# Kernel tuning notes

Measured on AMD Instinct MI355X. Metric: run time of the kernel, lower is better.

Reference implementation:

```python
import jax, jax.numpy as jnp
import numpy as np

# static config (levels=4, CDA=False branch -> self_attn_4, scale=4, f=False)
SHAPES = [(80, 80), (40, 40), (20, 20), (10, 10)]
D = 256; NH = 8; NL = 4; NP = 4; DFF = 1024; DH = D // NH
L = sum(h * w for h, w in SHAPES)  # 8500
B = 1


def layer_norm(x, g, b, eps=1e-5):
    m = jnp.mean(x, axis=-1, keepdims=True)
    v = jnp.mean((x - m) ** 2, axis=-1, keepdims=True)
    return (x - m) * jax.lax.rsqrt(v + eps) * g + b


def ms_deform_attn_core(value, loc, attn):
    # value: [B, L, NH, DH]; loc: [B, Lq, NH, NL, NP, 2] in [0,1]; attn: [B, Lq, NH, NL, NP]
    Bq, Lq = loc.shape[0], loc.shape[1]
    out = jnp.zeros((Bq, NH, Lq, DH), value.dtype)
    start = 0
    for lvl, (Hl, Wl) in enumerate(SHAPES):
        v = value[:, start:start + Hl * Wl]          # [B, HW, NH, DH]
        start += Hl * Wl
        v = v.transpose(0, 2, 1, 3)                  # [B, NH, HW, DH]
        ll = loc[:, :, :, lvl]                       # [B, Lq, NH, NP, 2]
        # grid_sample semantics: align_corners=False, padding_mode='zeros'
        x = ll[..., 0] * Wl - 0.5
        y = ll[..., 1] * Hl - 0.5
        x0 = jnp.floor(x); y0 = jnp.floor(y)
        acc = jnp.zeros((Bq, NH, Lq, NP, DH), value.dtype)
        for dy in (0, 1):
            for dx in (0, 1):
                xi = x0 + dx; yi = y0 + dy
                w = (1.0 - jnp.abs(x - xi)) * (1.0 - jnp.abs(y - yi))  # [B,Lq,NH,NP]
                valid = (xi >= 0) & (xi < Wl) & (yi >= 0) & (yi < Hl)
                xi_c = jnp.clip(xi, 0, Wl - 1).astype(jnp.int32)
                yi_c = jnp.clip(yi, 0, Hl - 1).astype(jnp.int32)
                lin = (yi_c * Wl + xi_c).transpose(0, 2, 1, 3).reshape(Bq, NH, Lq * NP)
                g = jnp.take_along_axis(v, lin[..., None], axis=2).reshape(Bq, NH, Lq, NP, DH)
                wv = (w * valid.astype(w.dtype)).transpose(0, 2, 1, 3)[..., None]
                acc = acc + g * wv
        aw = attn[:, :, :, lvl].transpose(0, 2, 1, 3)[..., None]  # [B,NH,Lq,NP,1]
        out = out + jnp.sum(acc * aw, axis=3)
    return out.transpose(0, 2, 1, 3).reshape(Bq, Lq, NH * DH)


def setup_inputs():
    key = jax.random.key(0)
    ks = jax.random.split(key, 24)
    s = 0.02
    d = {}
    d['src'] = jax.random.normal(ks[0], (B, L, D), jnp.float32)
    d['pos'] = jax.random.normal(ks[1], (B, L, D), jnp.float32)
    d['reference_points'] = jax.random.uniform(ks[2], (B, L, NL, 2), jnp.float32)
    d['spatial_shapes'] = jnp.array(SHAPES, jnp.int32)
    d['level_start_index'] = jnp.array(np.cumsum([0] + [h * w for h, w in SHAPES[:-1]]), jnp.int32)
    d['scale'] = 4
    # MSDeformAttn params
    d['Wo'] = jax.random.normal(ks[3], (D, NH * NL * NP * 2), jnp.float32) * s
    d['bo'] = jax.random.normal(ks[4], (NH * NL * NP * 2,), jnp.float32) * s
    d['Wa'] = jax.random.normal(ks[5], (D, NH * NL * NP), jnp.float32) * s
    d['ba'] = jax.random.normal(ks[6], (NH * NL * NP,), jnp.float32) * s
    d['Wv'] = jax.random.normal(ks[7], (D, D), jnp.float32) * s
    d['bv'] = jnp.zeros((D,), jnp.float32)
    d['Wout'] = jax.random.normal(ks[8], (D, D), jnp.float32) * s
    d['bout'] = jnp.zeros((D,), jnp.float32)
    # FFN + LayerNorms
    d['W1'] = jax.random.normal(ks[9], (D, DFF), jnp.float32) * s
    d['b1'] = jnp.zeros((DFF,), jnp.float32)
    d['W2'] = jax.random.normal(ks[10], (DFF, D), jnp.float32) * s
    d['b2'] = jnp.zeros((D,), jnp.float32)
    d['g1'] = jnp.ones((D,), jnp.float32); d['be1'] = jnp.zeros((D,), jnp.float32)
    d['g2'] = jnp.ones((D,), jnp.float32); d['be2'] = jnp.zeros((D,), jnp.float32)
    return d


def reference(src, pos, reference_points, spatial_shapes, level_start_index, scale,
              Wo, bo, Wa, ba, Wv, bv, Wout, bout, W1, b1, W2, b2, g1, be1, g2, be2):
    Bq, Lq, _ = src.shape
    q = src + pos  # with_pos_embed
    # sampling offsets & attention weights (softmax over levels*points)
    off = (q @ Wo + bo).reshape(Bq, Lq, NH, NL, NP, 2)
    attn = jax.nn.softmax((q @ Wa + ba).reshape(Bq, Lq, NH, NL * NP), axis=-1)
    attn = attn.reshape(Bq, Lq, NH, NL, NP)
    value = (src @ Wv + bv).reshape(Bq, L, NH, DH)
    # offset normalizer is (W, H) per level
    normalizer = jnp.stack([spatial_shapes[:, 1], spatial_shapes[:, 0]], -1).astype(src.dtype)
    loc = reference_points[:, :, None, :, None, :] + off / normalizer[None, None, None, :, None, :]
    src2 = ms_deform_attn_core(value, loc, attn) @ Wout + bout
    # residual + norm1 (dropout = eval identity)
    x = layer_norm(src + src2, g1, be1)
    # FFN
    ffn = jax.nn.relu(x @ W1 + b1) @ W2 + b2
    x = layer_norm(x + ffn, g2, be2)
    return x
```

## Files before the change

### kernel.cpp

```cpp
#include <hip/hip_runtime.h>
#include <hip/hip_bf16.h>
#include <string.h>

#define D 256
#define NH 8
#define DH 32
#define NL 4
#define NP 4
#define DFF 1024
#define LTOT 8500

typedef __bf16 bf16x8 __attribute__((ext_vector_type(8)));
typedef float floatx4 __attribute__((ext_vector_type(4)));

__device__ inline unsigned bpack(float a, float b) {
    __hip_bfloat16 ha = __float2bfloat16(a), hb = __float2bfloat16(b);
    unsigned short ua, ub;
    memcpy(&ua, &ha, 2); memcpy(&ub, &hb, 2);
    return (unsigned)ua | ((unsigned)ub << 16);
}

__device__ inline void gload16(const void* g, void* l) {
    __builtin_amdgcn_global_load_lds((const __attribute__((address_space(1))) void*)g,
                                     (__attribute__((address_space(3))) void*)l,
                                     16, 0, 0);
}

__global__ void transpose_all(const float* W0, const float* W1_, const float* W2_,
                              const float* W3, const float* W4, const float* W5,
                              __hip_bfloat16* T0, __hip_bfloat16* T1, __hip_bfloat16* T2,
                              __hip_bfloat16* T3, __hip_bfloat16* T4, __hip_bfloat16* T5,
                              const float* src, const float* pos,
                              __hip_bfloat16* qb, __hip_bfloat16* srcb) {
    int id = blockIdx.x;
    if (id >= 736) {
        int idx = (id - 736) * 2048 + threadIdx.x * 8;
        if (idx < LTOT * 256) {
            float4 s0 = *(const float4*)(src + idx);
            float4 s1 = *(const float4*)(src + idx + 4);
            float4 p0 = *(const float4*)(pos + idx);
            float4 p1 = *(const float4*)(pos + idx + 4);
            uint4 us, uq;
            us.x = bpack(s0.x, s0.y); us.y = bpack(s0.z, s0.w);
            us.z = bpack(s1.x, s1.y); us.w = bpack(s1.z, s1.w);
            uq.x = bpack(s0.x + p0.x, s0.y + p0.y); uq.y = bpack(s0.z + p0.z, s0.w + p0.w);
            uq.z = bpack(s1.x + p1.x, s1.y + p1.y); uq.w = bpack(s1.z + p1.z, s1.w + p1.w);
            *(uint4*)(srcb + idx) = us;
            *(uint4*)(qb + idx)  = uq;
        }
        return;
    }
    const int cum[7] = {0, 64, 96, 160, 224, 480, 736};
    int mi = 0;
    while (id >= cum[mi + 1]) mi++;
    int lid = id - cum[mi];
    const float* W; __hip_bfloat16* T; int K, N;
    switch (mi) {
        case 0: W = W0; T = T0; K = 256;  N = 256;  break;
        case 1: W = W1_; T = T1; K = 256; N = 128;  break;
        case 2: W = W2_; T = T2; K = 256; N = 256;  break;
        case 3: W = W3; T = T3; K = 256;  N = 256;  break;
        case 4: W = W4; T = T4; K = 256;  N = 1024; break;
        default: W = W5; T = T5; K = 1024; N = 256; break;
    }
    int ntx = N >> 5;
    int n0 = (lid % ntx) * 32, k0 = (lid / ntx) * 32;
    __shared__ float t[32][33];
    int tx = threadIdx.x & 31, ty = threadIdx.x >> 5;
#pragma unroll
    for (int i = 0; i < 32; i += 8)
        t[ty + i][tx] = W[(size_t)(k0 + ty + i) * N + n0 + tx];
    __syncthreads();
#pragma unroll
    for (int i = 0; i < 32; i += 8)
        T[(size_t)(n0 + ty + i) * K + k0 + tx] = __float2bfloat16(t[tx][ty + i]);
}

__global__ __launch_bounds__(256) void gemm_t(
    const __hip_bfloat16* __restrict__ A, const __hip_bfloat16* __restrict__ BT,
    const float* __restrict__ bias, float* __restrict__ Cf, __hip_bfloat16* __restrict__ Cb,
    int M, int N, int K, int relu) {
    constexpr int BM = 64, BN = 64, BK = 64;
    __shared__ __align__(16) __hip_bfloat16 sA[BM * BK];
    __shared__ __align__(16) __hip_bfloat16 sB[BN * BK];

    int tid = threadIdx.x, wave = tid >> 6, lane = tid & 63;
    int m0 = blockIdx.y * BM, n0 = blockIdx.x * BN;
    int wm = (wave >> 1) * 32, wn = (wave & 1) * 32;

    floatx4 acc[2][2];
#pragma unroll
    for (int i = 0; i < 2; i++)
#pragma unroll
        for (int j = 0; j < 2; j++)
#pragma unroll
            for (int e = 0; e < 4; e++) acc[i][j][e] = 0.f;

    int lrow = lane & 15, swz = lrow & 7;
    int scol = ((lane & 7) ^ (lane >> 3)) << 3;

    const __hip_bfloat16* aP[2];
    const __hip_bfloat16* bP[2];
#pragma unroll
    for (int i = 0; i < 2; i++) {
        int ra = m0 + i * 32 + wave * 8 + (lane >> 3); if (ra >= M) ra = M - 1;
        aP[i] = A + (size_t)ra * K + scol;
        int rb = n0 + i * 32 + wave * 8 + (lane >> 3);
        bP[i] = BT + (size_t)rb * K + scol;
    }
    int dOff = wave * 1024 + lane * 16;

    for (int k0 = 0; k0 < K; k0 += BK) {
#pragma unroll
        for (int i = 0; i < 2; i++) gload16(aP[i] + k0, (char*)sA + i * 4096 + dOff);
#pragma unroll
        for (int i = 0; i < 2; i++) gload16(bP[i] + k0, (char*)sB + i * 4096 + dOff);
        __syncthreads();
#pragma unroll
        for (int kk = 0; kk < 2; kk++) {
            int co = (((kk << 2) + (lane >> 4)) ^ swz) << 3;
            bf16x8 af[2], bfr[2];
#pragma unroll
            for (int tm = 0; tm < 2; tm++)
                af[tm] = *(const bf16x8*)(&sA[(wm + tm * 16 + lrow) * BK + co]);
#pragma unroll
            for (int tn = 0; tn < 2; tn++)
                bfr[tn] = *(const bf16x8*)(&sB[(wn + tn * 16 + lrow) * BK + co]);
#pragma unroll
            for (int tm = 0; tm < 2; tm++)
#pragma unroll
                for (int tn = 0; tn < 2; tn++)
                    acc[tm][tn] = __builtin_amdgcn_mfma_f32_16x16x32_bf16(af[tm], bfr[tn], acc[tm][tn], 0, 0, 0);
        }
        __syncthreads();
    }

    int lcol = lane & 15, lr4 = (lane >> 4) * 4;
#pragma unroll
    for (int tm = 0; tm < 2; tm++) {
#pragma unroll
        for (int i = 0; i < 4; i++) {
            int row = m0 + wm + tm * 16 + lr4 + i;
            if (row < M) {
#pragma unroll
                for (int tn = 0; tn < 2; tn++) {
                    int col = n0 + wn + tn * 16 + lcol;
                    float v = acc[tm][tn][i] + bias[col];
                    if (relu) v = fmaxf(v, 0.f);
                    if (Cf) Cf[(size_t)row * N + col] = v;
                    if (Cb) Cb[(size_t)row * N + col] = __float2bfloat16(v);
                }
            }
        }
    }
}

__global__ __launch_bounds__(256) void proj2(
    const __hip_bfloat16* __restrict__ qb, const __hip_bfloat16* __restrict__ srcb,
    const __hip_bfloat16* __restrict__ WoT, const __hip_bfloat16* __restrict__ WaT,
    const __hip_bfloat16* __restrict__ WvT,
    const float* __restrict__ bo, const float* __restrict__ ba, const float* __restrict__ bv,
    float* __restrict__ locb, float* __restrict__ attnb, __hip_bfloat16* __restrict__ valb,
    int M) {
    constexpr int BM = 64, BN = 64, BK = 64, K = 256;
    __shared__ __align__(16) __hip_bfloat16 sA[BM * BK];
    __shared__ __align__(16) __hip_bfloat16 sB[BN * BK];

    int n0 = blockIdx.x * BN;
    int m0 = blockIdx.y * BM;

    const __hip_bfloat16* BT;
    const __hip_bfloat16* A;
    const float* bias;
    int ncol0, Nout;
    float* Cf; __hip_bfloat16* Cb;
    if (n0 < 256)      { A = qb;   BT = WoT; bias = bo; ncol0 = n0;       Nout = 256; Cf = locb;  Cb = nullptr; }
    else if (n0 < 384) { A = qb;   BT = WaT; bias = ba; ncol0 = n0 - 256; Nout = 128; Cf = attnb; Cb = nullptr; }
    else               { A = srcb; BT = WvT; bias = bv; ncol0 = n0 - 384; Nout = 256; Cf = nullptr; Cb = valb; }

    int tid = threadIdx.x, wave = tid >> 6, lane = tid & 63;
    int wm = (wave >> 1) * 32, wn = (wave & 1) * 32;

    floatx4 acc[2][2];
#pragma unroll
    for (int i = 0; i < 2; i++)
#pragma unroll
        for (int j = 0; j < 2; j++)
#pragma unroll
            for (int e = 0; e < 4; e++) acc[i][j][e] = 0.f;

    int lrow = lane & 15, swz = lrow & 7;
    int scol = ((lane & 7) ^ (lane >> 3)) << 3;

    const __hip_bfloat16* aP[2];
    const __hip_bfloat16* bP[2];
#pragma unroll
    for (int i = 0; i < 2; i++) {
        int ra = m0 + i * 32 + wave * 8 + (lane >> 3); if (ra >= M) ra = M - 1;
        aP[i] = A + (size_t)ra * K + scol;
        int rb = ncol0 + i * 32 + wave * 8 + (lane >> 3);
        bP[i] = BT + (size_t)rb * K + scol;
    }
    int dOff = wave * 1024 + lane * 16;

    for (int k0 = 0; k0 < K; k0 += BK) {
#pragma unroll
        for (int i = 0; i < 2; i++) gload16(aP[i] + k0, (char*)sA + i * 4096 + dOff);
#pragma unroll
        for (int i = 0; i < 2; i++) gload16(bP[i] + k0, (char*)sB + i * 4096 + dOff);
        __syncthreads();
#pragma unroll
        for (int kk = 0; kk < 2; kk++) {
            int co = (((kk << 2) + (lane >> 4)) ^ swz) << 3;
            bf16x8 af[2], bfr[2];
#pragma unroll
            for (int tm = 0; tm < 2; tm++)
                af[tm] = *(const bf16x8*)(&sA[(wm + tm * 16 + lrow) * BK + co]);
#pragma unroll
            for (int tn = 0; tn < 2; tn++)
                bfr[tn] = *(const bf16x8*)(&sB[(wn + tn * 16 + lrow) * BK + co]);
#pragma unroll
            for (int tm = 0; tm < 2; tm++)
#pragma unroll
                for (int tn = 0; tn < 2; tn++)
                    acc[tm][tn] = __builtin_amdgcn_mfma_f32_16x16x32_bf16(af[tm], bfr[tn], acc[tm][tn], 0, 0, 0);
        }
        __syncthreads();
    }

    int lcol = lane & 15, lr4 = (lane >> 4) * 4;
#pragma unroll
    for (int tm = 0; tm < 2; tm++) {
#pragma unroll
        for (int i = 0; i < 4; i++) {
            int row = m0 + wm + tm * 16 + lr4 + i;
            if (row < M) {
#pragma unroll
                for (int tn = 0; tn < 2; tn++) {
                    int col = ncol0 + wn + tn * 16 + lcol;
                    float v = acc[tm][tn][i] + bias[col];
                    if (Cf) Cf[(size_t)row * Nout + col] = v;
                    else    Cb[(size_t)row * Nout + col] = __float2bfloat16(v);
                }
            }
        }
    }
}

__global__ __launch_bounds__(256) void deform(const __hip_bfloat16* __restrict__ value,
                                              const float* __restrict__ locraw,
                                              const float* __restrict__ logits,
                                              const float* __restrict__ refp,
                                              __hip_bfloat16* __restrict__ out) {
    __shared__ float wS[4][8][16][4];
    __shared__ int   aS[4][8][16][4];
    int tid = threadIdx.x;
    int q0 = blockIdx.x * 4;

    {
        int sub = tid >> 6, h = (tid >> 3) & 7, t8 = tid & 7;
        int q = q0 + sub;
        const float* lg = logits + q * 128 + h * 16;
        float l0 = lg[t8], l1 = lg[t8 + 8];
        float mx = fmaxf(l0, l1);
#pragma unroll
        for (int m = 1; m < 8; m <<= 1) mx = fmaxf(mx, __shfl_xor(mx, m, 64));
        float e0 = __expf(l0 - mx), e1 = __expf(l1 - mx);
        float s = e0 + e1;
#pragma unroll
        for (int m = 1; m < 8; m <<= 1) s += __shfl_xor(s, m, 64);
        float inv = 1.f / s;

        const int starts[4] = {0, 6400, 8000, 8400};
#pragma unroll
        for (int j = 0; j < 2; j++) {
            int pp = t8 + 8 * j;
            float a = (j ? e1 : e0) * inv;
            int l = pp >> 2;
            int Wl = 80 >> l;
            float nv = (float)Wl;
            float rx = refp[q * 8 + l * 2 + 0];
            float ry = refp[q * 8 + l * 2 + 1];
            float lx = rx + locraw[q * 256 + h * 32 + pp * 2 + 0] / nv;
            float ly = ry + locraw[q * 256 + h * 32 + pp * 2 + 1] / nv;
            float x = lx * nv - 0.5f;
            float y = ly * nv - 0.5f;
            float x0f = floorf(x), y0f = floorf(y);
            float fx = x - x0f, fy = y - y0f;
            int x0 = (int)x0f, y0 = (int)y0f;
            float wts[4] = {(1.f - fx) * (1.f - fy), fx * (1.f - fy),
                            (1.f - fx) * fy,         fx * fy};
            int st = starts[l];
#pragma unroll
            for (int t = 0; t < 4; t++) {
                int xi = x0 + (t & 1), yi = y0 + (t >> 1);
                bool valid = (xi >= 0) & (xi < Wl) & (yi >= 0) & (yi < Wl);
                int xc = min(max(xi, 0), Wl - 1), yc = min(max(yi, 0), Wl - 1);
                wS[sub][h][pp][t] = valid ? wts[t] * a : 0.f;
                aS[sub][h][pp][t] = (st + yc * Wl + xc) * 512 + h * 64;
            }
        }
    }
    __syncthreads();

    int sub = tid >> 6, h = (tid >> 3) & 7, l8 = tid & 7;
    int q = q0 + sub;
    const char* vb = (const char*)value;
    int lo = l8 * 8;
    float a0 = 0.f, a1 = 0.f, a2 = 0.f, a3 = 0.f;
#pragma unroll
    for (int p = 0; p < 16; p++) {
        floatx4 w = *(const floatx4*)&wS[sub][h][p][0];
        int4 av = *(const int4*)&aS[sub][h][p][0];
#pragma unroll
        for (int t = 0; t < 4; t++) {
            int ad = (t == 0) ? av.x : (t == 1) ? av.y : (t == 2) ? av.z : av.w;
            uint2 u = *(const uint2*)(vb + ad + lo);
            float wt = w[t];
            a0 += wt * __uint_as_float(u.x << 16);
            a1 += wt * __uint_as_float(u.x & 0xffff0000u);
            a2 += wt * __uint_as_float(u.y << 16);
            a3 += wt * __uint_as_float(u.y & 0xffff0000u);
        }
    }
    uint2 o;
    o.x = bpack(a0, a1);
    o.y = bpack(a2, a3);
    *(uint2*)((char*)out + q * 512 + h * 64 + l8 * 8) = o;
}

__global__ __launch_bounds__(512) void gemm_ln(
    const __hip_bfloat16* __restrict__ A, const __hip_bfloat16* __restrict__ BT,
    const float* __restrict__ bias, const float* __restrict__ resid,
    const float* __restrict__ g, const float* __restrict__ be,
    float* __restrict__ outf, __hip_bfloat16* __restrict__ outb,
    int M, int K) {
    constexpr int BM = 16, BK = 64;
    __shared__ __align__(16) __hip_bfloat16 sA[BM * BK];
    __shared__ __align__(16) __hip_bfloat16 sB[256 * BK];
    __shared__ float psum[8][16], psq[8][16], mS[16], rS[16];

    int tid = threadIdx.x;
    int wave = tid >> 6, lane = tid & 63;
    int m0 = blockIdx.x * BM;

    floatx4 acc[2];
#pragma unroll
    for (int j = 0; j < 2; j++)
#pragma unroll
        for (int e = 0; e < 4; e++) acc[j][e] = 0.f;

    int lrow = lane & 15, swz = lrow & 7;

    int scolA = ((lane & 7) ^ (lane >> 3)) << 3;
    int grA = m0 + wave * 8 + (lane >> 3); if (grA >= M) grA = M - 1;
    const __hip_bfloat16* aP = A + (size_t)grA * K + scolA;

    int scolB = ((tid & 7) ^ ((tid >> 3) & 7)) << 3;
    const __hip_bfloat16* bP[4];
#pragma unroll
    for (int i = 0; i < 4; i++)
        bP[i] = BT + (size_t)(i * 64 + (tid >> 3)) * K + scolB;

    for (int k0 = 0; k0 < K; k0 += BK) {
        if (wave < 2) gload16(aP + k0, (char*)sA + wave * 1024 + lane * 16);
#pragma unroll
        for (int i = 0; i < 4; i++) gload16(bP[i] + k0, (char*)sB + i * 8192 + tid * 16);
        __syncthreads();
#pragma unroll
        for (int kk = 0; kk < 2; kk++) {
            int co = (((kk << 2) + (lane >> 4)) ^ swz) << 3;
            bf16x8 af, bfr[2];
            af = *(const bf16x8*)(&sA[lrow * BK + co]);
#pragma unroll
            for (int tn = 0; tn < 2; tn++)
                bfr[tn] = *(const bf16x8*)(&sB[(wave * 32 + tn * 16 + lrow) * BK + co]);
#pragma unroll
            for (int tn = 0; tn < 2; tn++)
                acc[tn] = __builtin_amdgcn_mfma_f32_16x16x32_bf16(af, bfr[tn], acc[tn], 0, 0, 0);
        }
        __syncthreads();
    }

    int lcol = lane & 15, quad = lane >> 4;
    float v[2][4];
#pragma unroll
    for (int i = 0; i < 4; i++) {
        int row = quad * 4 + i;
        int grow = m0 + row; if (grow >= M) grow = M - 1;
#pragma unroll
        for (int tn = 0; tn < 2; tn++) {
            int col = wave * 32 + tn * 16 + lcol;
            v[tn][i] = acc[tn][i] + bias[col] + resid[(size_t)grow * 256 + col];
        }
    }

#pragma unroll
    for (int i = 0; i < 4; i++) {
        float s = 0.f, s2 = 0.f;
#pragma unroll
        for (int tn = 0; tn < 2; tn++) { float x = v[tn][i]; s += x; s2 += x * x; }
#pragma unroll
        for (int m = 1; m < 16; m <<= 1) {
            s  += __shfl_xor(s, m, 64);
            s2 += __shfl_xor(s2, m, 64);
        }
        if (lcol == 0) {
            int row = quad * 4 + i;
            psum[wave][row] = s;
            psq[wave][row]  = s2;
        }
    }
    __syncthreads();
    if (tid < 16) {
        float s = 0.f, s2 = 0.f;
#pragma unroll
        for (int w = 0; w < 8; w++) { s += psum[w][tid]; s2 += psq[w][tid]; }
        float m = s * (1.f / 256.f);
        float var = fmaxf(s2 * (1.f / 256.f) - m * m, 0.f);
        mS[tid] = m;
        rS[tid] = rsqrtf(var + 1e-5f);
    }
    __syncthreads();

#pragma unroll
    for (int i = 0; i < 4; i++) {
        int row = quad * 4 + i;
        int grow = m0 + row;
        if (grow < M) {
            float m = mS[row], r = rS[row];
#pragma unroll
            for (int tn = 0; tn < 2; tn++) {
                int col = wave * 32 + tn * 16 + lcol;
                float o = (v[tn][i] - m) * r * g[col] + be[col];
                outf[(size_t)grow * 256 + col] = o;
                if (outb) outb[(size_t)grow * 256 + col] = __float2bfloat16(o);
            }
        }
    }
}

extern "C" void kernel_launch(void* const* d_in, const int* in_sizes, int n_in,
                              void* d_out, int out_size, void* d_ws, size_t ws_size,
                              hipStream_t stream) {
    const float* src  = (const float*)d_in[0];
    const float* pos  = (const float*)d_in[1];
    const float* refp = (const float*)d_in[2];
    const float* Wo   = (const float*)d_in[6];
    const float* bo   = (const float*)d_in[7];
    const float* Wa   = (const float*)d_in[8];
    const float* ba   = (const float*)d_in[9];
    const float* Wv   = (const float*)d_in[10];
    const float* bv   = (const float*)d_in[11];
    const float* Wout = (const float*)d_in[12];
    const float* bout = (const float*)d_in[13];
    const float* W1   = (const float*)d_in[14];
    const float* b1   = (const float*)d_in[15];
    const float* W2   = (const float*)d_in[16];
    const float* b2   = (const float*)d_in[17];
    const float* g1   = (const float*)d_in[18];
    const float* be1  = (const float*)d_in[19];
    const float* g2   = (const float*)d_in[20];
    const float* be2  = (const float*)d_in[21];
    float* out = (float*)d_out;
    char* ws = (char*)d_ws;

    __hip_bfloat16* WoT   = (__hip_bfloat16*)(ws + 0);
    __hip_bfloat16* WaT   = (__hip_bfloat16*)(ws + 131072);
    __hip_bfloat16* WvT   = (__hip_bfloat16*)(ws + 196608);
    __hip_bfloat16* WoutT = (__hip_bfloat16*)(ws + 327680);
    __hip_bfloat16* W1T   = (__hip_bfloat16*)(ws + 458752);
    __hip_bfloat16* W2T   = (__hip_bfloat16*)(ws + 983040);
    float*          locb  = (float*)(ws + 1507328);
    float*          attnb = (float*)(ws + 10211328);
    __hip_bfloat16* valb  = (__hip_bfloat16*)(ws + 14563328);
    __hip_bfloat16* aob   = (__hip_bfloat16*)(ws + 18915328);
    float*          x1    = (float*)(ws + 23267328);
    __hip_bfloat16* x1b   = (__hip_bfloat16*)(ws + 31971328);
    __hip_bfloat16* hb    = (__hip_bfloat16*)(ws + 36323328);
    __hip_bfloat16* qb    = (__hip_bfloat16*)(ws + 36323328);
    __hip_bfloat16* srcb  = (__hip_bfloat16*)(ws + 36323328 + 4352000);

    transpose_all<<<736 + 1063, 256, 0, stream>>>(Wo, Wa, Wv, Wout, W1, W2,
                                                  WoT, WaT, WvT, WoutT, W1T, W2T,
                                                  src, pos, qb, srcb);

    proj2<<<dim3(10, 133), 256, 0, stream>>>(qb, srcb, WoT, WaT, WvT, bo, ba, bv,
                                             locb, attnb, valb, LTOT);

    deform<<<2125, 256, 0, stream>>>(valb, locb, attnb, refp, aob);

    gemm_ln<<<532, 512, 0, stream>>>(aob, WoutT, bout, src, g1, be1, x1, x1b, LTOT, 256);

    gemm_t<<<dim3(16, 133), 256, 0, stream>>>(x1b, W1T, b1, nullptr, hb, LTOT, 1024, 256, 1);

    gemm_ln<<<532, 512, 0, stream>>>(hb, W2T, b2, x1, g2, be2, out, nullptr, LTOT, 1024);
}
```

Measured before the change: 197.0 us.

## Fuse all stages into one cooperative persistent kernel with grid syncs

Replaces the six separate launches (transpose/convert, projection GEMM, deformable sampling, two GEMM+LayerNorm stages and the FFN GEMM) with a single cooperative kernel of 512-thread blocks. Stages are separated by grid.sync and blocks loop over work units. GEMM tiles change to 64x128 with 8 waves. The aim is to remove launch overhead and inter-kernel gaps. In exchange, grid-wide barriers, occupancy limited by the shared-memory union, and grid-stride imbalance may cost more than the launches they replace.

```diff
diff --git a/kernel.cpp b/kernel.cpp
--- a/kernel.cpp
+++ b/kernel.cpp
@@ -1,6 +1,9 @@
 #include <hip/hip_runtime.h>
 #include <hip/hip_bf16.h>
+#include <hip/hip_cooperative_groups.h>
 #include <string.h>
+
+namespace cg = cooperative_groups;
 
 #define D 256
 #define NH 8
@@ -26,67 +29,24 @@
                                      16, 0, 0);
 }
 
-__global__ void transpose_all(const float* W0, const float* W1_, const float* W2_,
-                              const float* W3, const float* W4, const float* W5,
-                              __hip_bfloat16* T0, __hip_bfloat16* T1, __hip_bfloat16* T2,
-                              __hip_bfloat16* T3, __hip_bfloat16* T4, __hip_bfloat16* T5,
-                              const float* src, const float* pos,
-                              __hip_bfloat16* qb, __hip_bfloat16* srcb) {
-    int id = blockIdx.x;
-    if (id >= 736) {
-        int idx = (id - 736) * 2048 + threadIdx.x * 8;
-        if (idx < LTOT * 256) {
-            float4 s0 = *(const float4*)(src + idx);
-            float4 s1 = *(const float4*)(src + idx + 4);
-            float4 p0 = *(const float4*)(pos + idx);
-            float4 p1 = *(const float4*)(pos + idx + 4);
-            uint4 us, uq;
-            us.x = bpack(s0.x, s0.y); us.y = bpack(s0.z, s0.w);
-            us.z = bpack(s1.x, s1.y); us.w = bpack(s1.z, s1.w);
-            uq.x = bpack(s0.x + p0.x, s0.y + p0.y); uq.y = bpack(s0.z + p0.z, s0.w + p0.w);
-            uq.z = bpack(s1.x + p1.x, s1.y + p1.y); uq.w = bpack(s1.z + p1.z, s1.w + p1.w);
-            *(uint4*)(srcb + idx) = us;
-            *(uint4*)(qb + idx)  = uq;
-        }
-        return;
-    }
-    const int cum[7] = {0, 64, 96, 160, 224, 480, 736};
-    int mi = 0;
-    while (id >= cum[mi + 1]) mi++;
-    int lid = id - cum[mi];
-    const float* W; __hip_bfloat16* T; int K, N;
-    switch (mi) {
-        case 0: W = W0; T = T0; K = 256;  N = 256;  break;
-        case 1: W = W1_; T = T1; K = 256; N = 128;  break;
-        case 2: W = W2_; T = T2; K = 256; N = 256;  break;
-        case 3: W = W3; T = T3; K = 256;  N = 256;  break;
-        case 4: W = W4; T = T4; K = 256;  N = 1024; break;
-        default: W = W5; T = T5; K = 1024; N = 256; break;
-    }
-    int ntx = N >> 5;
-    int n0 = (lid % ntx) * 32, k0 = (lid / ntx) * 32;
-    __shared__ float t[32][33];
-    int tx = threadIdx.x & 31, ty = threadIdx.x >> 5;
-#pragma unroll
-    for (int i = 0; i < 32; i += 8)
-        t[ty + i][tx] = W[(size_t)(k0 + ty + i) * N + n0 + tx];
-    __syncthreads();
-#pragma unroll
-    for (int i = 0; i < 32; i += 8)
-        T[(size_t)(n0 + ty + i) * K + k0 + tx] = __float2bfloat16(t[tx][ty + i]);
-}
-
-__global__ __launch_bounds__(256) void gemm_t(
-    const __hip_bfloat16* __restrict__ A, const __hip_bfloat16* __restrict__ BT,
-    const float* __restrict__ bias, float* __restrict__ Cf, __hip_bfloat16* __restrict__ Cb,
-    int M, int N, int K, int relu) {
-    constexpr int BM = 64, BN = 64, BK = 64;
-    __shared__ __align__(16) __hip_bfloat16 sA[BM * BK];
-    __shared__ __align__(16) __hip_bfloat16 sB[BN * BK];
-
+__device__ void gemm_64x128(char* smem,
+                            const __hip_bfloat16* A, const __hip_bfloat16* BT,
+                            int m0, int bRow0, int K, int M,
+                            const float* bias, int colOff, int ldOut,
+                            float* Cf, __hip_bfloat16* Cb, int relu) {
+    __hip_bfloat16* sA = (__hip_bfloat16*)smem;
+    __hip_bfloat16* sB = (__hip_bfloat16*)(smem + 8192);
     int tid = threadIdx.x, wave = tid >> 6, lane = tid & 63;
-    int m0 = blockIdx.y * BM, n0 = blockIdx.x * BN;
-    int wm = (wave >> 1) * 32, wn = (wave & 1) * 32;
+    int wm = (wave >> 2) * 32, wn = (wave & 3) * 32;
+    int lrow = lane & 15, swz = lrow & 7;
+    int scol = ((tid & 7) ^ ((tid >> 3) & 7)) << 3;
+
+    int ra = m0 + (tid >> 3); if (ra >= M) ra = M - 1;
+    const __hip_bfloat16* aP = A + (size_t)ra * K + scol;
+    const __hip_bfloat16* bP[2];
+#pragma unroll
+    for (int i = 0; i < 2; i++)
+        bP[i] = BT + (size_t)(bRow0 + i * 64 + (tid >> 3)) * K + scol;
 
     floatx4 acc[2][2];
 #pragma unroll
@@ -96,25 +56,11 @@
 #pragma unroll
             for (int e = 0; e < 4; e++) acc[i][j][e] = 0.f;
 
-    int lrow = lane & 15, swz = lrow & 7;
-    int scol = ((lane & 7) ^ (lane >> 3)) << 3;
-
-    const __hip_bfloat16* aP[2];
-    const __hip_bfloat16* bP[2];
-#pragma unroll
-    for (int i = 0; i < 2; i++) {
-        int ra = m0 + i * 32 + wave * 8 + (lane >> 3); if (ra >= M) ra = M - 1;
-        aP[i] = A + (size_t)ra * K + scol;
-        int rb = n0 + i * 32 + wave * 8 + (lane >> 3);
-        bP[i] = BT + (size_t)rb * K + scol;
-    }
-    int dOff = wave * 1024 + lane * 16;
-
-    for (int k0 = 0; k0 < K; k0 += BK) {
-#pragma unroll
-        for (int i = 0; i < 2; i++) gload16(aP[i] + k0, (char*)sA + i * 4096 + dOff);
-#pragma unroll
-        for (int i = 0; i < 2; i++) gload16(bP[i] + k0, (char*)sB + i * 4096 + dOff);
+    for (int k0 = 0; k0 < K; k0 += 64) {
+        gload16(aP + k0, smem + tid * 16);
+#pragma unroll
+        for (int i = 0; i < 2; i++)
+            gload16(bP[i] + k0, smem + 8192 + (i * 512 + tid) * 16);
         __syncthreads();
 #pragma unroll
         for (int kk = 0; kk < 2; kk++) {
@@ -122,10 +68,10 @@
             bf16x8 af[2], bfr[2];
 #pragma unroll
             for (int tm = 0; tm < 2; tm++)
-                af[tm] = *(const bf16x8*)(&sA[(wm + tm * 16 + lrow) * BK + co]);
+                af[tm] = *(const bf16x8*)(&sA[(wm + tm * 16 + lrow) * 64 + co]);
 #pragma unroll
             for (int tn = 0; tn < 2; tn++)
-                bfr[tn] = *(const bf16x8*)(&sB[(wn + tn * 16 + lrow) * BK + co]);
+                bfr[tn] = *(const bf16x8*)(&sB[(wn + tn * 16 + lrow) * 64 + co]);
 #pragma unroll
             for (int tm = 0; tm < 2; tm++)
 #pragma unroll
@@ -144,213 +90,38 @@
             if (row < M) {
 #pragma unroll
                 for (int tn = 0; tn < 2; tn++) {
-                    int col = n0 + wn + tn * 16 + lcol;
-                    float v = acc[tm][tn][i] + bias[col];
+                    int c = wn + tn * 16 + lcol;
+                    float v = acc[tm][tn][i] + bias[colOff + c];
                     if (relu) v = fmaxf(v, 0.f);
-                    if (Cf) Cf[(size_t)row * N + col] = v;
-                    if (Cb) Cb[(size_t)row * N + col] = __float2bfloat16(v);
+                    if (Cf) Cf[(size_t)row * ldOut + colOff + c] = v;
+                    else    Cb[(size_t)row * ldOut + colOff + c] = __float2bfloat16(v);
                 }
             }
         }
     }
 }
 
-__global__ __launch_bounds__(256) void proj2(
-    const __hip_bfloat16* __restrict__ qb, const __hip_bfloat16* __restrict__ srcb,
-    const __hip_bfloat16* __restrict__ WoT, const __hip_bfloat16* __restrict__ WaT,
-    const __hip_bfloat16* __restrict__ WvT,
-    const float* __restrict__ bo, const float* __restrict__ ba, const float* __restrict__ bv,
-    float* __restrict__ locb, float* __restrict__ attnb, __hip_bfloat16* __restrict__ valb,
-    int M) {
-    constexpr int BM = 64, BN = 64, BK = 64, K = 256;
-    __shared__ __align__(16) __hip_bfloat16 sA[BM * BK];
-    __shared__ __align__(16) __hip_bfloat16 sB[BN * BK];
-
-    int n0 = blockIdx.x * BN;
-    int m0 = blockIdx.y * BM;
-
-    const __hip_bfloat16* BT;
-    const __hip_bfloat16* A;
-    const float* bias;
-    int ncol0, Nout;
-    float* Cf; __hip_bfloat16* Cb;
-    if (n0 < 256)      { A = qb;   BT = WoT; bias = bo; ncol0 = n0;       Nout = 256; Cf = locb;  Cb = nullptr; }
-    else if (n0 < 384) { A = qb;   BT = WaT; bias = ba; ncol0 = n0 - 256; Nout = 128; Cf = attnb; Cb = nullptr; }
-    else               { A = srcb; BT = WvT; bias = bv; ncol0 = n0 - 384; Nout = 256; Cf = nullptr; Cb = valb; }
+__device__ void gemm_ln_dev(char* smem,
+                            const __hip_bfloat16* A, const __hip_bfloat16* BT,
+                            const float* bias, const float* resid,
+                            const float* g, const float* be,
+                            float* outf, __hip_bfloat16* outb,
+                            int m0, int M, int K) {
+    __hip_bfloat16* sA = (__hip_bfloat16*)smem;
+    __hip_bfloat16* sB = (__hip_bfloat16*)(smem + 2048);
+    float* psum = (float*)(smem + 34816);
+    float* psq  = (float*)(smem + 35328);
+    float* mS   = (float*)(smem + 35840);
+    float* rS   = (float*)(smem + 35904);
 
     int tid = threadIdx.x, wave = tid >> 6, lane = tid & 63;
-    int wm = (wave >> 1) * 32, wn = (wave & 1) * 32;
-
-    floatx4 acc[2][2];
-#pragma unroll
-    for (int i = 0; i < 2; i++)
-#pragma unroll
-        for (int j = 0; j < 2; j++)
-#pragma unroll
-            for (int e = 0; e < 4; e++) acc[i][j][e] = 0.f;
-
     int lrow = lane & 15, swz = lrow & 7;
-    int scol = ((lane & 7) ^ (lane >> 3)) << 3;
-
-    const __hip_bfloat16* aP[2];
-    const __hip_bfloat16* bP[2];
-#pragma unroll
-    for (int i = 0; i < 2; i++) {
-        int ra = m0 + i * 32 + wave * 8 + (lane >> 3); if (ra >= M) ra = M - 1;
-        aP[i] = A + (size_t)ra * K + scol;
-        int rb = ncol0 + i * 32 + wave * 8 + (lane >> 3);
-        bP[i] = BT + (size_t)rb * K + scol;
-    }
-    int dOff = wave * 1024 + lane * 16;
-
-    for (int k0 = 0; k0 < K; k0 += BK) {
-#pragma unroll
-        for (int i = 0; i < 2; i++) gload16(aP[i] + k0, (char*)sA + i * 4096 + dOff);
-#pragma unroll
-        for (int i = 0; i < 2; i++) gload16(bP[i] + k0, (char*)sB + i * 4096 + dOff);
-        __syncthreads();
-#pragma unroll
-        for (int kk = 0; kk < 2; kk++) {
-            int co = (((kk << 2) + (lane >> 4)) ^ swz) << 3;
-            bf16x8 af[2], bfr[2];
-#pragma unroll
-            for (int tm = 0; tm < 2; tm++)
-                af[tm] = *(const bf16x8*)(&sA[(wm + tm * 16 + lrow) * BK + co]);
-#pragma unroll
-            for (int tn = 0; tn < 2; tn++)
-                bfr[tn] = *(const bf16x8*)(&sB[(wn + tn * 16 + lrow) * BK + co]);
-#pragma unroll
-            for (int tm = 0; tm < 2; tm++)
-#pragma unroll
-                for (int tn = 0; tn < 2; tn++)
-                    acc[tm][tn] = __builtin_amdgcn_mfma_f32_16x16x32_bf16(af[tm], bfr[tn], acc[tm][tn], 0, 0, 0);
-        }
-        __syncthreads();
-    }
-
-    int lcol = lane & 15, lr4 = (lane >> 4) * 4;
-#pragma unroll
-    for (int tm = 0; tm < 2; tm++) {
-#pragma unroll
-        for (int i = 0; i < 4; i++) {
-            int row = m0 + wm + tm * 16 + lr4 + i;
-            if (row < M) {
-#pragma unroll
-                for (int tn = 0; tn < 2; tn++) {
-                    int col = ncol0 + wn + tn * 16 + lcol;
-                    float v = acc[tm][tn][i] + bias[col];
-                    if (Cf) Cf[(size_t)row * Nout + col] = v;
-                    else    Cb[(size_t)row * Nout + col] = __float2bfloat16(v);
-                }
-            }
-        }
-    }
-}
-
-__global__ __launch_bounds__(256) void deform(const __hip_bfloat16* __restrict__ value,
-                                              const float* __restrict__ locraw,
-                                              const float* __restrict__ logits,
-                                              const float* __restrict__ refp,
-                                              __hip_bfloat16* __restrict__ out) {
-    __shared__ float wS[4][8][16][4];
-    __shared__ int   aS[4][8][16][4];
-    int tid = threadIdx.x;
-    int q0 = blockIdx.x * 4;
-
-    {
-        int sub = tid >> 6, h = (tid >> 3) & 7, t8 = tid & 7;
-        int q = q0 + sub;
-        const float* lg = logits + q * 128 + h * 16;
-        float l0 = lg[t8], l1 = lg[t8 + 8];
-        float mx = fmaxf(l0, l1);
-#pragma unroll
-        for (int m = 1; m < 8; m <<= 1) mx = fmaxf(mx, __shfl_xor(mx, m, 64));
-        float e0 = __expf(l0 - mx), e1 = __expf(l1 - mx);
-        float s = e0 + e1;
-#pragma unroll
-        for (int m = 1; m < 8; m <<= 1) s += __shfl_xor(s, m, 64);
-        float inv = 1.f / s;
-
-        const int starts[4] = {0, 6400, 8000, 8400};
-#pragma unroll
-        for (int j = 0; j < 2; j++) {
-            int pp = t8 + 8 * j;
-            float a = (j ? e1 : e0) * inv;
-            int l = pp >> 2;
-            int Wl = 80 >> l;
-            float nv = (float)Wl;
-            float rx = refp[q * 8 + l * 2 + 0];
-            float ry = refp[q * 8 + l * 2 + 1];
-            float lx = rx + locraw[q * 256 + h * 32 + pp * 2 + 0] / nv;
-            float ly = ry + locraw[q * 256 + h * 32 + pp * 2 + 1] / nv;
-            float x = lx * nv - 0.5f;
-            float y = ly * nv - 0.5f;
-            float x0f = floorf(x), y0f = floorf(y);
-            float fx = x - x0f, fy = y - y0f;
-            int x0 = (int)x0f, y0 = (int)y0f;
-            float wts[4] = {(1.f - fx) * (1.f - fy), fx * (1.f - fy),
-                            (1.f - fx) * fy,         fx * fy};
-            int st = starts[l];
-#pragma unroll
-            for (int t = 0; t < 4; t++) {
-                int xi = x0 + (t & 1), yi = y0 + (t >> 1);
-                bool valid = (xi >= 0) & (xi < Wl) & (yi >= 0) & (yi < Wl);
-                int xc = min(max(xi, 0), Wl - 1), yc = min(max(yi, 0), Wl - 1);
-                wS[sub][h][pp][t] = valid ? wts[t] * a : 0.f;
-                aS[sub][h][pp][t] = (st + yc * Wl + xc) * 512 + h * 64;
-            }
-        }
-    }
-    __syncthreads();
-
-    int sub = tid >> 6, h = (tid >> 3) & 7, l8 = tid & 7;
-    int q = q0 + sub;
-    const char* vb = (const char*)value;
-    int lo = l8 * 8;
-    float a0 = 0.f, a1 = 0.f, a2 = 0.f, a3 = 0.f;
-#pragma unroll
-    for (int p = 0; p < 16; p++) {
-        floatx4 w = *(const floatx4*)&wS[sub][h][p][0];
-        int4 av = *(const int4*)&aS[sub][h][p][0];
-#pragma unroll
-        for (int t = 0; t < 4; t++) {
-            int ad = (t == 0) ? av.x : (t == 1) ? av.y : (t == 2) ? av.z : av.w;
-            uint2 u = *(const uint2*)(vb + ad + lo);
-            float wt = w[t];
-            a0 += wt * __uint_as_float(u.x << 16);
-            a1 += wt * __uint_as_float(u.x & 0xffff0000u);
-            a2 += wt * __uint_as_float(u.y << 16);
-            a3 += wt * __uint_as_float(u.y & 0xffff0000u);
-        }
-    }
-    uint2 o;
-    o.x = bpack(a0, a1);
-    o.y = bpack(a2, a3);
-    *(uint2*)((char*)out + q * 512 + h * 64 + l8 * 8) = o;
-}
-
-__global__ __launch_bounds__(512) void gemm_ln(
-    const __hip_bfloat16* __restrict__ A, const __hip_bfloat16* __restrict__ BT,
-    const float* __restrict__ bias, const float* __restrict__ resid,
-    const float* __restrict__ g, const float* __restrict__ be,
-    float* __restrict__ outf, __hip_bfloat16* __restrict__ outb,
-    int M, int K) {
-    constexpr int BM = 16, BK = 64;
-    __shared__ __align__(16) __hip_bfloat16 sA[BM * BK];
-    __shared__ __align__(16) __hip_bfloat16 sB[256 * BK];
-    __shared__ float psum[8][16], psq[8][16], mS[16], rS[16];
-
-    int tid = threadIdx.x;
-    int wave = tid >> 6, lane = tid & 63;
-    int m0 = blockIdx.x * BM;
 
     floatx4 acc[2];
 #pragma unroll
     for (int j = 0; j < 2; j++)
 #pragma unroll
         for (int e = 0; e < 4; e++) acc[j][e] = 0.f;
-
-    int lrow = lane & 15, swz = lrow & 7;
 
     int scolA = ((lane & 7) ^ (lane >> 3)) << 3;
     int grA = m0 + wave * 8 + (lane >> 3); if (grA >= M) grA = M - 1;
@@ -362,19 +133,20 @@
     for (int i = 0; i < 4; i++)
         bP[i] = BT + (size_t)(i * 64 + (tid >> 3)) * K + scolB;
 
-    for (int k0 = 0; k0 < K; k0 += BK) {
-        if (wave < 2) gload16(aP + k0, (char*)sA + wave * 1024 + lane * 16);
-#pragma unroll
-        for (int i = 0; i < 4; i++) gload16(bP[i] + k0, (char*)sB + i * 8192 + tid * 16);
+    for (int k0 = 0; k0 < K; k0 += 64) {
+        if (wave < 2) gload16(aP + k0, smem + wave * 1024 + lane * 16);
+#pragma unroll
+        for (int i = 0; i < 4; i++)
+            gload16(bP[i] + k0, smem + 2048 + i * 8192 + tid * 16);
         __syncthreads();
 #pragma unroll
         for (int kk = 0; kk < 2; kk++) {
             int co = (((kk << 2) + (lane >> 4)) ^ swz) << 3;
-            bf16x8 af, bfr[2];
-            af = *(const bf16x8*)(&sA[lrow * BK + co]);
+            bf16x8 af = *(const bf16x8*)(&sA[lrow * 64 + co]);
+            bf16x8 bfr[2];
 #pragma unroll
             for (int tn = 0; tn < 2; tn++)
-                bfr[tn] = *(const bf16x8*)(&sB[(wave * 32 + tn * 16 + lrow) * BK + co]);
+                bfr[tn] = *(const bf16x8*)(&sB[(wave * 32 + tn * 16 + lrow) * 64 + co]);
 #pragma unroll
             for (int tn = 0; tn < 2; tn++)
                 acc[tn] = __builtin_amdgcn_mfma_f32_16x16x32_bf16(af, bfr[tn], acc[tn], 0, 0, 0);
@@ -407,15 +179,15 @@
         }
         if (lcol == 0) {
             int row = quad * 4 + i;
-            psum[wave][row] = s;
-            psq[wave][row]  = s2;
+            psum[wave * 16 + row] = s;
+            psq[wave * 16 + row]  = s2;
         }
     }
     __syncthreads();
     if (tid < 16) {
         float s = 0.f, s2 = 0.f;
 #pragma unroll
-        for (int w = 0; w < 8; w++) { s += psum[w][tid]; s2 += psq[w][tid]; }
+        for (int w = 0; w < 8; w++) { s += psum[w * 16 + tid]; s2 += psq[w * 16 + tid]; }
         float m = s * (1.f / 256.f);
         float var = fmaxf(s2 * (1.f / 256.f) - m * m, 0.f);
         mS[tid] = m;
@@ -438,6 +210,184 @@
             }
         }
     }
+    __syncthreads();
+}
+
+__global__ void mega(
+    const float* src, const float* pos, const float* refp,
+    const float* Wo, const float* bo, const float* Wa, const float* ba,
+    const float* Wv, const float* bv, const float* Wout, const float* bout,
+    const float* W1, const float* b1, const float* W2, const float* b2,
+    const float* g1, const float* be1, const float* g2, const float* be2,
+    float* out, char* ws) {
+    __shared__ __align__(16) char smem[35968];
+    int tid = threadIdx.x;
+    cg::grid_group grid = cg::this_grid();
+
+    __hip_bfloat16* WoT   = (__hip_bfloat16*)(ws + 0);
+    __hip_bfloat16* WaT   = (__hip_bfloat16*)(ws + 131072);
+    __hip_bfloat16* WvT   = (__hip_bfloat16*)(ws + 196608);
+    __hip_bfloat16* WoutT = (__hip_bfloat16*)(ws + 327680);
+    __hip_bfloat16* W1T   = (__hip_bfloat16*)(ws + 458752);
+    __hip_bfloat16* W2T   = (__hip_bfloat16*)(ws + 983040);
+    float*          locb  = (float*)(ws + 1507328);
+    float*          attnb = (float*)(ws + 10211328);
+    __hip_bfloat16* valb  = (__hip_bfloat16*)(ws + 14563328);
+    __hip_bfloat16* aob   = (__hip_bfloat16*)(ws + 18915328);
+    float*          x1    = (float*)(ws + 23267328);
+    __hip_bfloat16* x1b   = (__hip_bfloat16*)(ws + 31971328);
+    __hip_bfloat16* qb    = (__hip_bfloat16*)(ws + 36323328);
+    __hip_bfloat16* srcb  = (__hip_bfloat16*)(ws + 40675328);
+    __hip_bfloat16* hb    = (__hip_bfloat16*)(ws + 45027328);
+
+    for (int u = blockIdx.x; u < 1268; u += gridDim.x) {
+        if (u < 736) {
+            const int cum[7] = {0, 64, 96, 160, 224, 480, 736};
+            int mi = 0;
+            while (u >= cum[mi + 1]) mi++;
+            int lid = u - cum[mi];
+            const float* W; __hip_bfloat16* T; int K, N;
+            switch (mi) {
+                case 0: W = Wo;   T = WoT;   K = 256;  N = 256;  break;
+                case 1: W = Wa;   T = WaT;   K = 256;  N = 128;  break;
+                case 2: W = Wv;   T = WvT;   K = 256;  N = 256;  break;
+                case 3: W = Wout; T = WoutT; K = 256;  N = 256;  break;
+                case 4: W = W1;   T = W1T;   K = 256;  N = 1024; break;
+                default: W = W2;  T = W2T;   K = 1024; N = 256;  break;
+            }
+            int ntx = N >> 5;
+            int n0 = (lid % ntx) * 32, k0 = (lid / ntx) * 32;
+            float* t = (float*)smem;
+            int tx = tid & 31, ty = tid >> 5;
+#pragma unroll
+            for (int i = 0; i < 32; i += 16)
+                t[(ty + i) * 33 + tx] = W[(size_t)(k0 + ty + i) * N + n0 + tx];
+            __syncthreads();
+#pragma unroll
+            for (int i = 0; i < 32; i += 16)
+                T[(size_t)(n0 + ty + i) * K + k0 + tx] = __float2bfloat16(t[tx * 33 + ty + i]);
+            __syncthreads();
+        } else {
+            int idx = (u - 736) * 4096 + tid * 8;
+            if (idx < LTOT * 256) {
+                float4 s0 = *(const float4*)(src + idx);
+                float4 s1 = *(const float4*)(src + idx + 4);
+                float4 p0 = *(const float4*)(pos + idx);
+                float4 p1 = *(const float4*)(pos + idx + 4);
+                uint4 us, uq;
+                us.x = bpack(s0.x, s0.y); us.y = bpack(s0.z, s0.w);
+                us.z = bpack(s1.x, s1.y); us.w = bpack(s1.z, s1.w);
+                uq.x = bpack(s0.x + p0.x, s0.y + p0.y); uq.y = bpack(s0.z + p0.z, s0.w + p0.w);
+                uq.z = bpack(s1.x + p1.x, s1.y + p1.y); uq.w = bpack(s1.z + p1.z, s1.w + p1.w);
+                *(uint4*)(srcb + idx) = us;
+                *(uint4*)(qb + idx)  = uq;
+            }
+        }
+    }
+    grid.sync();
+
+    for (int u = blockIdx.x; u < 665; u += gridDim.x) {
+        int n0 = (u % 5) * 128, m0 = (u / 5) * 64;
+        const __hip_bfloat16* Ap; const __hip_bfloat16* BTp;
+        const float* bias; int ncol0, Nout; float* Cf; __hip_bfloat16* Cb;
+        if (n0 < 256)      { Ap = qb;   BTp = WoT; bias = bo; ncol0 = n0;       Nout = 256; Cf = locb;  Cb = nullptr; }
+        else if (n0 < 384) { Ap = qb;   BTp = WaT; bias = ba; ncol0 = 0;        Nout = 128; Cf = attnb; Cb = nullptr; }
+        else               { Ap = srcb; BTp = WvT; bias = bv; ncol0 = n0 - 384; Nout = 256; Cf = nullptr; Cb = valb; }
+        gemm_64x128(smem, Ap, BTp, m0, ncol0, 256, LTOT, bias, ncol0, Nout, Cf, Cb, 0);
+    }
+    grid.sync();
+
+    for (int u = blockIdx.x; u < 1063; u += gridDim.x) {
+        float* wS = (float*)smem;
+        int*   aS = (int*)(smem + 16384);
+        int sub = tid >> 6, h = (tid >> 3) & 7, t8 = tid & 7;
+        int q = u * 8 + sub; if (q >= LTOT) q = LTOT - 1;
+        {
+            const float* lg = attnb + q * 128 + h * 16;
+            float l0 = lg[t8], l1 = lg[t8 + 8];
+            float mx = fmaxf(l0, l1);
+#pragma unroll
+            for (int m = 1; m < 8; m <<= 1) mx = fmaxf(mx, __shfl_xor(mx, m, 64));
+            float e0 = __expf(l0 - mx), e1 = __expf(l1 - mx);
+            float s = e0 + e1;
+#pragma unroll
+            for (int m = 1; m < 8; m <<= 1) s += __shfl_xor(s, m, 64);
+            float inv = 1.f / s;
+
+            const int starts[4] = {0, 6400, 8000, 8400};
+#pragma unroll
+            for (int j = 0; j < 2; j++) {
+                int pp = t8 + 8 * j;
+                float a = (j ? e1 : e0) * inv;
+                int l = pp >> 2;
+                int Wl = 80 >> l;
+                float nv = (float)Wl;
+                float rx = refp[q * 8 + l * 2 + 0];
+                float ry = refp[q * 8 + l * 2 + 1];
+                float lx = rx + locb[q * 256 + h * 32 + pp * 2 + 0] / nv;
+                float ly = ry + locb[q * 256 + h * 32 + pp * 2 + 1] / nv;
+                float x = lx * nv - 0.5f;
+                float y = ly * nv - 0.5f;
+                float x0f = floorf(x), y0f = floorf(y);
+                float fx = x - x0f, fy = y - y0f;
+                int x0 = (int)x0f, y0 = (int)y0f;
+                float wts[4] = {(1.f - fx) * (1.f - fy), fx * (1.f - fy),
+                                (1.f - fx) * fy,         fx * fy};
+                int st = starts[l];
+#pragma unroll
+                for (int t = 0; t < 4; t++) {
+                    int xi = x0 + (t & 1), yi = y0 + (t >> 1);
+                    bool valid = (xi >= 0) & (xi < Wl) & (yi >= 0) & (yi < Wl);
+                    int xc = min(max(xi, 0), Wl - 1), yc = min(max(yi, 0), Wl - 1);
+                    int base = ((sub * 8 + h) * 16 + pp) * 4 + t;
+                    wS[base] = valid ? wts[t] * a : 0.f;
+                    aS[base] = (st + yc * Wl + xc) * 512 + h * 64;
+                }
+            }
+        }
+        __syncthreads();
+        {
+            int l8 = tid & 7;
+            const char* vb = (const char*)valb;
+            int lo = l8 * 8;
+            float a0 = 0.f, a1 = 0.f, a2 = 0.f, a3 = 0.f;
+#pragma unroll
+            for (int p = 0; p < 16; p++) {
+                int base = ((sub * 8 + h) * 16 + p) * 4;
+                floatx4 w = *(const floatx4*)&wS[base];
+                int4 av = *(const int4*)&aS[base];
+#pragma unroll
+                for (int t = 0; t < 4; t++) {
+                    int ad = (t == 0) ? av.x : (t == 1) ? av.y : (t == 2) ? av.z : av.w;
+                    uint2 uu = *(const uint2*)(vb + ad + lo);
+                    float wt = w[t];
+                    a0 += wt * __uint_as_float(uu.x << 16);
+                    a1 += wt * __uint_as_float(uu.x & 0xffff0000u);
+                    a2 += wt * __uint_as_float(uu.y << 16);
+                    a3 += wt * __uint_as_float(uu.y & 0xffff0000u);
+                }
+            }
+            uint2 o;
+            o.x = bpack(a0, a1);
+            o.y = bpack(a2, a3);
+            *(uint2*)((char*)aob + (size_t)q * 512 + h * 64 + l8 * 8) = o;
+        }
+        __syncthreads();
+    }
+    grid.sync();
+
+    for (int u = blockIdx.x; u < 532; u += gridDim.x)
+        gemm_ln_dev(smem, aob, WoutT, bout, src, g1, be1, x1, x1b, u * 16, LTOT, 256);
+    grid.sync();
+
+    for (int u = blockIdx.x; u < 1064; u += gridDim.x) {
+        int n0 = (u & 7) * 128, m0 = (u >> 3) * 64;
+        gemm_64x128(smem, x1b, W1T, m0, n0, 256, LTOT, b1, n0, 1024, nullptr, hb, 1);
+    }
+    grid.sync();
+
+    for (int u = blockIdx.x; u < 532; u += gridDim.x)
+        gemm_ln_dev(smem, hb, W2T, b2, x1, g2, be2, out, nullptr, u * 16, LTOT, 1024);
 }
 
 extern "C" void kernel_launch(void* const* d_in, const int* in_sizes, int n_in,
@@ -465,34 +415,22 @@
     float* out = (float*)d_out;
     char* ws = (char*)d_ws;
 
-    __hip_bfloat16* WoT   = (__hip_bfloat16*)(ws + 0);
-    __hip_bfloat16* WaT   = (__hip_bfloat16*)(ws + 131072);
-    __hip_bfloat16* WvT   = (__hip_bfloat16*)(ws + 196608);
-    __hip_bfloat16* WoutT = (__hip_bfloat16*)(ws + 327680);
-    __hip_bfloat16* W1T   = (__hip_bfloat16*)(ws + 458752);
-    __hip_bfloat16* W2T   = (__hip_bfloat16*)(ws + 983040);
-    float*          locb  = (float*)(ws + 1507328);
-    float*          attnb = (float*)(ws + 10211328);
-    __hip_bfloat16* valb  = (__hip_bfloat16*)(ws + 14563328);
-    __hip_bfloat16* aob   = (__hip_bfloat16*)(ws + 18915328);
-    float*          x1    = (float*)(ws + 23267328);
-    __hip_bfloat16* x1b   = (__hip_bfloat16*)(ws + 31971328);
-    __hip_bfloat16* hb    = (__hip_bfloat16*)(ws + 36323328);
-    __hip_bfloat16* qb    = (__hip_bfloat16*)(ws + 36323328);
-    __hip_bfloat16* srcb  = (__hip_bfloat16*)(ws + 36323328 + 4352000);
-
-    transpose_all<<<736 + 1063, 256, 0, stream>>>(Wo, Wa, Wv, Wout, W1, W2,
-                                                  WoT, WaT, WvT, WoutT, W1T, W2T,
-                                                  src, pos, qb, srcb);
-
-    proj2<<<dim3(10, 133), 256, 0, stream>>>(qb, srcb, WoT, WaT, WvT, bo, ba, bv,
-                                             locb, attnb, valb, LTOT);
-
-    deform<<<2125, 256, 0, stream>>>(valb, locb, attnb, refp, aob);
-
-    gemm_ln<<<532, 512, 0, stream>>>(aob, WoutT, bout, src, g1, be1, x1, x1b, LTOT, 256);
-
-    gemm_t<<<dim3(16, 133), 256, 0, stream>>>(x1b, W1T, b1, nullptr, hb, LTOT, 1024, 256, 1);
-
-    gemm_ln<<<532, 512, 0, stream>>>(hb, W2T, b2, x1, g2, be2, out, nullptr, LTOT, 1024);
-}
+    static int nblk = 0;
+    if (nblk == 0) {
+        int bpc = 0;
+        hipOccupancyMaxActiveBlocksPerMultiprocessor(&bpc, mega, 512, 0);
+        if (bpc < 1) bpc = 1;
+        nblk = bpc * 256;
+        if (nblk > 1064) nblk = 1064;
+    }
+
+    void* args[] = {
+        (void*)&src, (void*)&pos, (void*)&refp,
+        (void*)&Wo, (void*)&bo, (void*)&Wa, (void*)&ba,
+        (void*)&Wv, (void*)&bv, (void*)&Wout, (void*)&bout,
+        (void*)&W1, (void*)&b1, (void*)&W2, (void*)&b2,
+        (void*)&g1, (void*)&be1, (void*)&g2, (void*)&be2,
+        (void*)&out, (void*)&ws
+    };
+    hipLaunchCooperativeKernel((void*)mega, dim3(nblk), dim3(512), args, 0, stream);
+}
```

Measured after the change: 465.1 us. 136% more time.
